# Performance work log

Measured on AMD Instinct MI355X. Metric: run time of the kernel, lower is better.

The kernel has to match this reference:

```python
import jax, jax.numpy as jnp
import numpy as np

NUM_HEADS = 16
HEAD_DIM = 64
NUM_BUCKETS = 32
MAX_DIST = 128
EPS = 1e-5
SCALE = HEAD_DIM ** -0.5


def layer_norm(x, g, b):
    m = jnp.mean(x, axis=-1, keepdims=True)
    v = jnp.mean(jnp.square(x - m), axis=-1, keepdims=True)
    return (x - m) * jax.lax.rsqrt(v + EPS) * g + b


def rel_pos_bias(emb, num_q, num_k):
    # T5-style relative position bucketing (non-causal, bidirectional halves)
    i, j = num_q, num_k
    q_pos = jnp.arange(j - i, j)
    k_pos = jnp.arange(j)
    rel = k_pos[None, :] - q_pos[:, None]  # [i, j]
    nb = NUM_BUCKETS // 2
    ret = (rel >= 0).astype(jnp.int32) * nb
    n = jnp.abs(rel)
    max_exact = nb // 2
    val_large = max_exact + (
        jnp.log(jnp.maximum(n, 1).astype(jnp.float32) / max_exact)
        / np.log(MAX_DIST / max_exact) * (nb - max_exact)
    ).astype(jnp.int32)
    val_large = jnp.minimum(val_large, nb - 1)
    bucket = ret + jnp.where(n < max_exact, n, val_large)
    bias = emb[bucket]                       # [i, j, h]
    return jnp.transpose(bias, (2, 0, 1))[None]  # [1, h, i, j]


def attention(x, ctx, ng, nbv, ncg, ncb, wq, wkv, wo, bo, rel_emb):
    b, n, _ = x.shape
    m = ctx.shape[1]
    xn = layer_norm(x, ng, nbv)
    cn = layer_norm(ctx, ncg, ncb)
    q = xn @ wq                              # [b, n, mid]
    kv = cn @ wkv                            # [b, m, 2*mid]
    k, v = jnp.split(kv, 2, axis=-1)
    def heads(t, L):
        return t.reshape(b, L, NUM_HEADS, HEAD_DIM).transpose(0, 2, 1, 3)
    q, k, v = heads(q, n), heads(k, m), heads(v, m)
    sim = jnp.einsum('bhnd,bhmd->bhnm', q, k)
    sim = (sim + rel_pos_bias(rel_emb, n, m)) * SCALE  # bias added pre-scale (faithful)
    attn = jax.nn.softmax(sim, axis=-1)
    out = jnp.einsum('bhnm,bhmd->bhnd', attn, v)
    out = out.transpose(0, 2, 1, 3).reshape(b, n, NUM_HEADS * HEAD_DIM)
    return out @ wo + bo


def setup_inputs() -> dict:
    key = jax.random.key(0)
    ks = jax.random.split(key, 20)
    F, MID, CF = 1024, NUM_HEADS * HEAD_DIM, 1024
    w = lambda k, shape, s=0.02: jax.random.normal(k, shape, jnp.float32) * s
    inp = {
        'x': jax.random.normal(ks[0], (2, 2048, F), jnp.float32),
        'context': jax.random.normal(ks[1], (2, 512, CF), jnp.float32),
        # self-attention params
        'sa_norm_g': 1.0 + w(ks[2], (F,), 0.1), 'sa_norm_b': w(ks[3], (F,), 0.1),
        'sa_normc_g': 1.0 + w(ks[4], (F,), 0.1), 'sa_normc_b': w(ks[5], (F,), 0.1),
        'sa_wq': w(ks[6], (F, MID)), 'sa_wkv': w(ks[7], (F, 2 * MID)),
        'sa_wo': w(ks[8], (MID, F)), 'sa_bo': w(ks[9], (F,), 0.01),
        'sa_rel': w(ks[10], (NUM_BUCKETS, NUM_HEADS), 0.1),
        # cross-attention params
        'ca_norm_g': 1.0 + w(ks[11], (F,), 0.1), 'ca_norm_b': w(ks[12], (F,), 0.1),
        'ca_normc_g': 1.0 + w(ks[13], (CF,), 0.1), 'ca_normc_b': w(ks[14], (CF,), 0.1),
        'ca_wq': w(ks[15], (F, MID)), 'ca_wkv': w(ks[16], (CF, 2 * MID)),
        'ca_wo': w(ks[17], (MID, F)), 'ca_bo': w(ks[18], (F,), 0.01),
        'ca_rel': w(ks[19], (NUM_BUCKETS, NUM_HEADS), 0.1),
    }
    return inp


def reference(x, context,
              sa_norm_g, sa_norm_b, sa_normc_g, sa_normc_b,
              sa_wq, sa_wkv, sa_wo, sa_bo, sa_rel,
              ca_norm_g, ca_norm_b, ca_normc_g, ca_normc_b,
              ca_wq, ca_wkv, ca_wo, ca_bo, ca_rel):
    # self-attention (context = x, norm_context applied to x)
    x = attention(x, x, sa_norm_g, sa_norm_b, sa_normc_g, sa_normc_b,
                  sa_wq, sa_wkv, sa_wo, sa_bo, sa_rel) + x
    # cross-attention with residual
    x = attention(x, context, ca_norm_g, ca_norm_b, ca_normc_g, ca_normc_b,
                  ca_wq, ca_wkv, ca_wo, ca_bo, ca_rel) + x
    return x
```

## Files before the change

### kernel.cpp

```cpp
#include <hip/hip_runtime.h>
#include <hip/hip_bf16.h>

typedef __hip_bfloat16 bf16;
typedef __attribute__((ext_vector_type(8))) short bf16x8;
typedef __attribute__((ext_vector_type(4))) float f32x4;

__device__ __forceinline__ float b2f(bf16 v) { return __bfloat162float(v); }
__device__ __forceinline__ bf16 f2b(float v) { return __float2bfloat16(v); }

__device__ __forceinline__ float ldx(const void* p, size_t i, bool isb) {
    return isb ? b2f(((const bf16*)p)[i]) : ((const float*)p)[i];
}
__device__ __forceinline__ void stx(void* p, size_t i, bool isb, float v) {
    if (isb) ((bf16*)p)[i] = f2b(v);
    else     ((float*)p)[i] = v;
}
__device__ __forceinline__ void ldx8(const void* p, size_t i, bool isb, float* o) {
    if (isb) {
        const bf16x8 v = *(const bf16x8*)((const bf16*)p + i);
#pragma unroll
        for (int j = 0; j < 8; j++) o[j] = b2f(((const bf16*)&v)[j]);
    } else {
        const float4 v0 = *(const float4*)((const float*)p + i);
        const float4 v1 = *(const float4*)((const float*)p + i + 4);
        o[0]=v0.x; o[1]=v0.y; o[2]=v0.z; o[3]=v0.w;
        o[4]=v1.x; o[5]=v1.y; o[6]=v1.z; o[7]=v1.w;
    }
}

__global__ void sniff_kernel(const void* __restrict__ x, int* __restrict__ flag) {
    const unsigned* w = (const unsigned*)x;
    const int t = threadIdx.x;
    int cnt = 0;
#pragma unroll
    for (int i = 0; i < 4; i++) {
        const unsigned word = w[t * 4 + i];
        const int e = (word >> 23) & 0xFF;
        cnt += (e >= 192) ? 1 : 0;
    }
    __shared__ int red[4];
#pragma unroll
    for (int o = 32; o > 0; o >>= 1) cnt += __shfl_down(cnt, o);
    if ((t & 63) == 0) red[t >> 6] = cnt;
    __syncthreads();
    if (t == 0) flag[0] = ((red[0] + red[1] + red[2] + red[3]) >= 512) ? 1 : 0;
}

__global__ void wconv8_kernel(const void* __restrict__ Wq,
                              const void* __restrict__ Wkv,
                              const void* __restrict__ Wo,
                              const void* __restrict__ Wq2,
                              const void* __restrict__ Wkv2,
                              const void* __restrict__ Wo2,
                              bf16* __restrict__ WTq, bf16* __restrict__ WTkv,
                              bf16* __restrict__ WTo,
                              bf16* __restrict__ WTq2, bf16* __restrict__ WTkv2,
                              bf16* __restrict__ WTo2,
                              const int* __restrict__ flagp) {
    const bool isb = (*flagp != 0);
    const int z = blockIdx.z;
    const int zz = z & 3;
    const bool ca = z >= 4;
    const void* W = ca ? ((zz == 0) ? Wq2 : (zz == 3) ? Wo2 : Wkv2)
                       : ((zz == 0) ? Wq  : (zz == 3) ? Wo  : Wkv);
    bf16* Wt      = ca ? ((zz == 0) ? WTq2 : (zz == 3) ? WTo2 : WTkv2)
                       : ((zz == 0) ? WTq  : (zz == 3) ? WTo  : WTkv);
    const int N   = (zz == 1 || zz == 2) ? 2048 : 1024;
    const int K = 1024;
    __shared__ float T[64][65];
    const int n0 = blockIdx.x * 64 + ((zz == 2) ? 1024 : 0);
    const int k0 = blockIdx.y * 64;
    const int t = threadIdx.x;
    const int rr = t >> 3, c8 = (t & 7) * 8;
#pragma unroll
    for (int i = 0; i < 2; i++) {
        const int row = rr + i * 32;
        float v[8];
        ldx8(W, (size_t)(k0 + row) * N + n0 + c8, isb, v);
#pragma unroll
        for (int j = 0; j < 8; j++) T[row][c8 + j] = v[j];
    }
    __syncthreads();
#pragma unroll
    for (int i = 0; i < 2; i++) {
        const int row = rr + i * 32;
        bf16x8 ov;
#pragma unroll
        for (int j = 0; j < 8; j++) ((bf16*)&ov)[j] = f2b(T[c8 + j][row]);
        *(bf16x8*)(Wt + (size_t)(n0 + row) * K + k0 + c8) = ov;
    }
}

__global__ void ln_dual_kernel(const void* __restrict__ in, size_t in_off, long in_bs,
                               int in_ext,
                               const void* __restrict__ g1, const void* __restrict__ b1,
                               const void* __restrict__ g2, const void* __restrict__ b2,
                               bf16* __restrict__ out1, bf16* __restrict__ out2,
                               long out_bs, const int* __restrict__ flagp) {
    const int F = 1024;
    const bool isb = (*flagp != 0);
    const bool inb = in_ext ? isb : true;
    const int row = blockIdx.x;
    const int z = blockIdx.z;
    const int t = threadIdx.x;
    const size_t base = in_off + (size_t)z * in_bs + (size_t)row * F;
    const size_t obase = (size_t)z * out_bs + (size_t)row * F;

    float v[4];
    float s = 0.f;
#pragma unroll
    for (int i = 0; i < 4; i++) { v[i] = ldx(in, base + t + 256 * i, inb); s += v[i]; }

    __shared__ float red1[4];
    __shared__ float red2[4];
#pragma unroll
    for (int o = 32; o > 0; o >>= 1) s += __shfl_down(s, o);
    if ((t & 63) == 0) red1[t >> 6] = s;
    __syncthreads();
    const float mean = (red1[0] + red1[1] + red1[2] + red1[3]) * (1.0f / F);

    float ss = 0.f;
#pragma unroll
    for (int i = 0; i < 4; i++) { float d = v[i] - mean; ss += d * d; }
#pragma unroll
    for (int o = 32; o > 0; o >>= 1) ss += __shfl_down(ss, o);
    if ((t & 63) == 0) red2[t >> 6] = ss;
    __syncthreads();
    const float var = (red2[0] + red2[1] + red2[2] + red2[3]) * (1.0f / F);
    const float rn = rsqrtf(var + 1e-5f);

#pragma unroll
    for (int i = 0; i < 4; i++) {
        const int idx = t + 256 * i;
        const float nv = (v[i] - mean) * rn;
        out1[obase + idx] = f2b(nv * ldx(g1, idx, isb) + ldx(b1, idx, isb));
        if (out2) out2[obase + idx] = f2b(nv * ldx(g2, idx, isb) + ldx(b2, idx, isb));
    }
}

struct GArgs {
    const bf16* A; const bf16* Bt; void* C;
    const void* bias; const void* res;
    bf16* kb0; bf16* kb1;
    int c_ext, res_ext, N, mode, zsplit, zrows, nbx, nby;
};

__global__ __launch_bounds__(256) void gemm_fused(GArgs ga, GArgs gb, GArgs gc,
                                                  const int* __restrict__ flagp) {
    int bx = (int)blockIdx.x;
    GArgs g;
    if (bx < ga.nbx) { g = ga; }
    else if (bx < ga.nbx + gb.nbx) { g = gb; bx -= ga.nbx; }
    else { g = gc; bx -= ga.nbx + gb.nbx; }
    const int by = (int)blockIdx.y;
    if (by >= g.nby) return;

    const int K = 1024;
    const bool isb = (*flagp != 0);

    __shared__ bf16 As[128][72];
    __shared__ bf16 Bs[128][72];

    const int t = threadIdx.x;
    const int w = t >> 6, lane = t & 63, li = lane & 15, quad = lane >> 4;
    const int wm = (w & 1) * 64, wn = (w >> 1) * 64;
    const int bm = by * 128, bn = bx * 128;

    f32x4 acc[4][4];
#pragma unroll
    for (int mi = 0; mi < 4; mi++)
#pragma unroll
        for (int ni = 0; ni < 4; ni++)
#pragma unroll
            for (int r = 0; r < 4; r++) acc[mi][ni][r] = 0.f;

    for (int k0 = 0; k0 < K; k0 += 64) {
#pragma unroll
        for (int c = 0; c < 4; c++) {
            const int d = c * 256 + t;
            const int row = d >> 3, ch = (d & 7) * 8;
            *(bf16x8*)&As[row][ch] = *(const bf16x8*)(g.A + (size_t)(bm + row) * K + k0 + ch);
            *(bf16x8*)&Bs[row][ch] = *(const bf16x8*)(g.Bt + (size_t)(bn + row) * K + k0 + ch);
        }
        __syncthreads();
#pragma unroll
        for (int kc = 0; kc < 2; kc++) {
            bf16x8 af[4], bfr[4];
#pragma unroll
            for (int i = 0; i < 4; i++) {
                af[i]  = *(const bf16x8*)&As[wm + i * 16 + li][kc * 32 + quad * 8];
                bfr[i] = *(const bf16x8*)&Bs[wn + i * 16 + li][kc * 32 + quad * 8];
            }
#pragma unroll
            for (int mi = 0; mi < 4; mi++)
#pragma unroll
                for (int ni = 0; ni < 4; ni++)
                    acc[mi][ni] = __builtin_amdgcn_mfma_f32_16x16x32_bf16(
                        af[mi], bfr[ni], acc[mi][ni], 0, 0, 0);
        }
        __syncthreads();
    }

    if (g.mode == 1) {
#pragma unroll
        for (int mi = 0; mi < 4; mi++)
#pragma unroll
            for (int r = 0; r < 4; r++) {
                const int row = bm + wm + mi * 16 + quad * 4 + r;
                bf16* kb = (row < g.zsplit) ? g.kb0 : g.kb1;
                const int lrow = (row < g.zsplit) ? row : row - g.zsplit;
#pragma unroll
                for (int ni = 0; ni < 4; ni++) {
                    const int col = bn + wn + ni * 16 + li;
                    const float v = acc[mi][ni][r];
                    if (col < 1024)
                        kb[(size_t)lrow * 1024 + col] = f2b(v);
                    else
                        kb[(size_t)1024 * g.zrows + (size_t)(col - 1024) * g.zrows + lrow] = f2b(v);
                }
            }
        return;
    }

#pragma unroll
    for (int mi = 0; mi < 4; mi++)
#pragma unroll
        for (int r = 0; r < 4; r++) {
            const int row = bm + wm + mi * 16 + quad * 4 + r;
#pragma unroll
            for (int ni = 0; ni < 4; ni++) {
                const int col = bn + wn + ni * 16 + li;
                float v = acc[mi][ni][r];
                if (g.bias) v += ldx(g.bias, col, isb);
                if (g.res)  v += ldx(g.res, (size_t)row * g.N + col, g.res_ext ? isb : true);
                stx(g.C, (size_t)row * g.N + col, g.c_ext ? isb : true, v);
            }
        }
}

__global__ __launch_bounds__(256) void gemm_mfma(
    const bf16* __restrict__ A, long a_bs, const void* __restrict__ W,
    void* __restrict__ C, size_t c_off, long c_bs, int c_ext,
    const void* __restrict__ bias,
    const void* __restrict__ res, size_t res_off, long res_bs, int res_ext,
    int K, int N, int mode, int R,
    bf16* __restrict__ kb0, bf16* __restrict__ kb1,
    const int* __restrict__ flagp) {

    const bool isb = (*flagp != 0);
    const bool resb = res_ext ? isb : true;
    const bool cb = c_ext ? isb : true;
    const int z = blockIdx.z;

    const bf16* Az = A + (size_t)z * a_bs;
    const size_t coz = c_off + (size_t)z * c_bs;
    const size_t roz = res_off + (size_t)z * res_bs;

    __shared__ bf16 As[64][72];
    __shared__ bf16 Bs[64][72];

    const int t = threadIdx.x;
    const int w = t >> 6, lane = t & 63, li = lane & 15, quad = lane >> 4;
    const int wm = (w & 1) * 32, wn = (w >> 1) * 32;
    const int bm = blockIdx.y * 64, bn = blockIdx.x * 64;

    f32x4 acc[2][2];
#pragma unroll
    for (int mi = 0; mi < 2; mi++)
#pragma unroll
        for (int ni = 0; ni < 2; ni++)
#pragma unroll
            for (int r = 0; r < 4; r++) acc[mi][ni][r] = 0.f;

    for (int k0 = 0; k0 < K; k0 += 64) {
#pragma unroll
        for (int c = 0; c < 2; c++) {
            const int lin = t * 16 + c * 8;
            const int row = lin >> 6, kk = lin & 63;
            *(bf16x8*)&As[row][kk] = *(const bf16x8*)(Az + (size_t)(bm + row) * K + k0 + kk);
        }
#pragma unroll
        for (int c = 0; c < 2; c++) {
            const int lin = t * 16 + c * 8;
            const int kk = lin >> 6, n0 = lin & 63;
            float v[8];
            ldx8(W, (size_t)(k0 + kk) * N + bn + n0, isb, v);
            const int st = t & 7;
#pragma unroll
            for (int i = 0; i < 8; i++) {
                const int ii = (i + st) & 7;
                Bs[n0 + ii][kk] = f2b(v[ii]);
            }
        }
        __syncthreads();
#pragma unroll
        for (int kc = 0; kc < 2; kc++) {
            bf16x8 af[2], bfr[2];
#pragma unroll
            for (int mi = 0; mi < 2; mi++)
                af[mi] = *(const bf16x8*)&As[wm + mi * 16 + li][kc * 32 + quad * 8];
#pragma unroll
            for (int ni = 0; ni < 2; ni++)
                bfr[ni] = *(const bf16x8*)&Bs[wn + ni * 16 + li][kc * 32 + quad * 8];
#pragma unroll
            for (int mi = 0; mi < 2; mi++)
#pragma unroll
                for (int ni = 0; ni < 2; ni++)
                    acc[mi][ni] = __builtin_amdgcn_mfma_f32_16x16x32_bf16(
                        af[mi], bfr[ni], acc[mi][ni], 0, 0, 0);
        }
        __syncthreads();
    }

    if (mode == 1) {
        bf16* kb = z ? kb1 : kb0;
#pragma unroll
        for (int mi = 0; mi < 2; mi++)
#pragma unroll
            for (int r = 0; r < 4; r++) {
                const int row = bm + wm + mi * 16 + quad * 4 + r;
#pragma unroll
                for (int ni = 0; ni < 2; ni++) {
                    const int col = bn + wn + ni * 16 + li;
                    const float v = acc[mi][ni][r];
                    if (col < 1024)
                        kb[(size_t)row * 1024 + col] = f2b(v);
                    else
                        kb[(size_t)1024 * R + (size_t)(col - 1024) * R + row] = f2b(v);
                }
            }
        return;
    }

#pragma unroll
    for (int mi = 0; mi < 2; mi++)
#pragma unroll
        for (int r = 0; r < 4; r++) {
            const int row = bm + wm + mi * 16 + quad * 4 + r;
#pragma unroll
            for (int ni = 0; ni < 2; ni++) {
                const int col = bn + wn + ni * 16 + li;
                float v = acc[mi][ni][r];
                if (bias) v += ldx(bias, col, isb);
                if (res)  v += ldx(res, roz + (size_t)row * N + col, resb);
                stx(C, coz + (size_t)row * N + col, cb, v);
            }
        }
}

__global__ __launch_bounds__(64) void attn_flash(
    const bf16* __restrict__ qb, const bf16* __restrict__ kv0,
    const bf16* __restrict__ kv1,
    const void* __restrict__ rel_emb, bf16* __restrict__ out,
    long qo_bs, long out_bs, int m, int rel_off, const int* __restrict__ flagp) {

    const float SC = 0.125f * 1.44269504f;
    const bool isb = (*flagp != 0);
    const int id = blockIdx.x;
    const int xcd = id & 7;
    const int slot = id >> 3;
    const int c = (slot >> 6) * 8 + xcd;
    const int h = c & 15, z = c >> 4;
    const int q0 = (slot & 63) * 32;
    const int t = threadIdx.x;
    const int li = t & 15, quad = t >> 4;

    const bf16* qz = qb + (size_t)z * qo_bs;
    bf16* oz = out + (size_t)z * out_bs;
    const bf16* kb = z ? kv1 : kv0;
    const bf16* vtb = kb + (size_t)m * 1024;

    __shared__ float bias_s[32];
    __shared__ float tab[2080];
    __shared__ bf16 Ps[2][16][40];

    if (t < 32) bias_s[t] = ldx(rel_emb, t * 16 + h, isb) * SC - 40.0f;
    __syncthreads();

    const int tsz = m + 31;
    for (int i = t; i < tsz; i += 64) {
        const int rel = i - 31 - q0 + rel_off;
        const int ab = rel < 0 ? -rel : rel;
        int bucket = rel >= 0 ? 16 : 0;
        if (ab < 8) {
            bucket += ab;
        } else {
            const int p = 31 - __clz(ab);
            const int k2 = 2 * p + ((ab * ab >= (1 << (2 * p + 1))) ? 1 : 0);
            const int val = k2 + 2;
            bucket += (val > 15) ? 15 : val;
        }
        tab[i] = bias_s[bucket];
    }
    __syncthreads();

    bf16x8 aq[2][2];
#pragma unroll
    for (int g = 0; g < 2; g++)
#pragma unroll
        for (int kc = 0; kc < 2; kc++)
            aq[g][kc] = *(const bf16x8*)(qz + (size_t)(q0 + g * 16 + li) * 1024
                                         + h * 64 + kc * 32 + quad * 8);

    bf16x8 ones;
#pragma unroll
    for (int j = 0; j < 8; j++) ((short*)&ones)[j] = 0x3F80;

    f32x4 o[2][4], lac[2];
#pragma unroll
    for (int g = 0; g < 2; g++) {
#pragma unroll
        for (int r = 0; r < 4; r++) lac[g][r] = 0.f;
#pragma unroll
        for (int nb = 0; nb < 4; nb++)
#pragma unroll
            for (int r = 0; r < 4; r++) o[g][nb][r] = 0.f;
    }

#define LOADKV(KF, VF, J)                                                      \
    {                                                                          \
        _Pragma("unroll")                                                      \
        for (int nb = 0; nb < 2; nb++)                                         \
            _Pragma("unroll")                                                  \
            for (int kc = 0; kc < 2; kc++)                                     \
                KF[nb * 2 + kc] = *(const bf16x8*)(                            \
                    kb + (size_t)((J) + nb * 16 + li) * 1024 + h * 64          \
                    + kc * 32 + quad * 8);                                     \
        _Pragma("unroll")                                                      \
        for (int nb = 0; nb < 4; nb++)                                         \
            VF[nb] = *(const bf16x8*)(                                         \
                vtb + (size_t)(h * 64 + nb * 16 + li) * m + (J) + quad * 8);   \
    }

#define ABODY(KF, VF, J0)                                                      \
    {                                                                          \
        _Pragma("unroll")                                                      \
        for (int g = 0; g < 2; g++) {                                          \
            f32x4 s[2];                                                        \
            _Pragma("unroll")                                                  \
            for (int nb = 0; nb < 2; nb++) {                                   \
                f32x4 a;                                                       \
                _Pragma("unroll")                                              \
                for (int r = 0; r < 4; r++) a[r] = 0.f;                        \
                _Pragma("unroll")                                              \
                for (int kc = 0; kc < 2; kc++)                                 \
                    a = __builtin_amdgcn_mfma_f32_16x16x32_bf16(               \
                        aq[g][kc], KF[nb * 2 + kc], a, 0, 0, 0);               \
                s[nb] = a;                                                     \
            }                                                                  \
            _Pragma("unroll")                                                  \
            for (int nb = 0; nb < 2; nb++)                                     \
                _Pragma("unroll")                                              \
                for (int r = 0; r < 4; r++) {                                  \
                    const int ti = (J0) + nb * 16 + li + 31                    \
                                   - (g * 16 + quad * 4 + r);                  \
                    s[nb][r] = exp2f(fmaf(s[nb][r], SC, tab[ti]));             \
                }                                                              \
            _Pragma("unroll")                                                  \
            for (int nb = 0; nb < 2; nb++)                                     \
                _Pragma("unroll")                                              \
                for (int r = 0; r < 4; r++)                                    \
                    Ps[g][quad * 4 + r][nb * 16 + li] = f2b(s[nb][r]);         \
            const bf16x8 ap = *(const bf16x8*)&Ps[g][li][quad * 8];            \
            _Pragma("unroll")                                                  \
            for (int nb = 0; nb < 4; nb++)                                     \
                o[g][nb] = __builtin_amdgcn_mfma_f32_16x16x32_bf16(            \
                    ap, VF[nb], o[g][nb], 0, 0, 0);                            \
            lac[g] = __builtin_amdgcn_mfma_f32_16x16x32_bf16(                  \
                ap, ones, lac[g], 0, 0, 0);                                    \
        }                                                                      \
    }

    bf16x8 kA[4], vA[4], kB[4], vB[4];
    LOADKV(kA, vA, 0);
    for (int j0 = 0; j0 < m; j0 += 64) {
        LOADKV(kB, vB, j0 + 32);
        ABODY(kA, vA, j0);
        const int jn = (j0 + 64 < m) ? (j0 + 64) : 0;
        LOADKV(kA, vA, jn);
        ABODY(kB, vB, j0 + 32);
    }

#undef LOADKV
#undef ABODY

#pragma unroll
    for (int g = 0; g < 2; g++)
#pragma unroll
        for (int r = 0; r < 4; r++) {
            const float inv = 1.0f / lac[g][r];
            const int qi = q0 + g * 16 + quad * 4 + r;
#pragma unroll
            for (int nb = 0; nb < 4; nb++)
                oz[(size_t)qi * 1024 + h * 64 + nb * 16 + li] = f2b(o[g][nb][r] * inv);
        }
}

extern "C" void kernel_launch(void* const* d_in, const int* in_sizes, int n_in,
                              void* d_out, int out_size, void* d_ws, size_t ws_size,
                              hipStream_t stream) {
    const long M1 = 1024 * 1024;
    const long M2 = 2 * 1024 * 1024;
    const long M4 = 4 * 1024 * 1024;
    if (ws_size < 24u * 1024 * 1024 + 256) return;

    const void* x      = d_in[0];
    const void* ctx    = d_in[1];
    const void* sa_ng  = d_in[2];
    const void* sa_nb  = d_in[3];
    const void* sa_ncg = d_in[4];
    const void* sa_ncb = d_in[5];
    const void* sa_wq  = d_in[6];
    const void* sa_wkv = d_in[7];
    const void* sa_wo  = d_in[8];
    const void* sa_bo  = d_in[9];
    const void* sa_rel = d_in[10];
    const void* ca_ng  = d_in[11];
    const void* ca_nb  = d_in[12];
    const void* ca_ncg = d_in[13];
    const void* ca_ncb = d_in[14];
    const void* ca_wq  = d_in[15];
    const void* ca_wkv = d_in[16];
    const void* ca_wo  = d_in[17];
    const void* ca_bo  = d_in[18];
    const void* ca_rel = d_in[19];

    int* flag = (int*)d_ws;
    bf16* F_A = (bf16*)((char*)d_ws + 256);
    bf16* F_B = F_A + M4;
    bf16* F_C = F_B + M4;
    bf16* WT  = F_C + M4;
    bf16* F_X = WT + M4;
    bf16* F_Y = F_X + M4;
    bf16* WT2 = F_Y + 3 * M1;
    bf16* qd  = (bf16*)d_out;

    sniff_kernel<<<1, 256, 0, stream>>>(x, flag);

    if (ws_size >= 56u * 1024 * 1024 + 256) {
        bf16* WTq  = WT;
        bf16* WTkv = WT + M1;
        bf16* WTo  = WT + 3 * M1;
        bf16* WT2q  = WT2;
        bf16* WT2kv = WT2 + M1;
        bf16* WT2o  = WT2 + 3 * M1;
        bf16* CAK0 = F_Y + M1;
        bf16* CAK1 = F_Y + 2 * M1;
        GArgs gz = {};

        wconv8_kernel<<<dim3(16, 16, 8), 256, 0, stream>>>(
            sa_wq, sa_wkv, sa_wo, ca_wq, ca_wkv, ca_wo,
            WTq, WTkv, WTo, WT2q, WT2kv, WT2o, flag);
        ln_dual_kernel<<<dim3(2048, 1, 2), 256, 0, stream>>>(
            x, 0, M2, 1, sa_ng, sa_nb, sa_ncg, sa_ncb, F_X, F_B, M2, flag);
        ln_dual_kernel<<<dim3(512, 1, 2), 256, 0, stream>>>(
            ctx, 0, 512 * 1024, 1, ca_ncg, ca_ncb, nullptr, nullptr,
            F_Y, nullptr, 512 * 1024, flag);

        {
            GArgs gq = {};
            gq.A = F_X; gq.Bt = WTq; gq.C = qd;
            gq.N = 1024; gq.nbx = 8; gq.nby = 32;
            GArgs gkv = {};
            gkv.A = F_B; gkv.Bt = WTkv;
            gkv.N = 2048; gkv.mode = 1; gkv.zsplit = 2048; gkv.zrows = 2048;
            gkv.kb0 = F_A; gkv.kb1 = F_C; gkv.nbx = 16; gkv.nby = 32;
            GArgs gca = {};
            gca.A = F_Y; gca.Bt = WT2kv;
            gca.N = 2048; gca.mode = 1; gca.zsplit = 512; gca.zrows = 512;
            gca.kb0 = CAK0; gca.kb1 = CAK1; gca.nbx = 16; gca.nby = 8;
            gemm_fused<<<dim3(40, 32), 256, 0, stream>>>(gq, gkv, gca, flag);
        }

        attn_flash<<<dim3(2048), 64, 0, stream>>>(
            qd, F_A, F_C, sa_rel, qd, M2, M2, 2048, 0, flag);
        {
            GArgs go = {};
            go.A = qd; go.Bt = WTo; go.C = F_B;
            go.bias = sa_bo; go.res = x; go.res_ext = 1;
            go.N = 1024; go.nbx = 8; go.nby = 32;
            gemm_fused<<<dim3(8, 32), 256, 0, stream>>>(go, gz, gz, flag);
        }

        ln_dual_kernel<<<dim3(2048, 1, 2), 256, 0, stream>>>(
            F_B, 0, M2, 0, ca_ng, ca_nb, nullptr, nullptr, F_X, nullptr, M2, flag);
        {
            GArgs gq = {};
            gq.A = F_X; gq.Bt = WT2q; gq.C = qd;
            gq.N = 1024; gq.nbx = 8; gq.nby = 32;
            gemm_fused<<<dim3(8, 32), 256, 0, stream>>>(gq, gz, gz, flag);
        }
        attn_flash<<<dim3(2048), 64, 0, stream>>>(
            qd, CAK0, CAK1, ca_rel, F_C, M2, M2, 512, 1536, flag);
        {
            GArgs go = {};
            go.A = F_C; go.Bt = WT2o; go.C = d_out; go.c_ext = 1;
            go.bias = ca_bo; go.res = F_B;
            go.N = 1024; go.nbx = 8; go.nby = 32;
            gemm_fused<<<dim3(8, 32), 256, 0, stream>>>(go, gz, gz, flag);
        }
        return;
    }

    ln_dual_kernel<<<dim3(2048, 1, 2), 256, 0, stream>>>(
        x, 0, M2, 1, sa_ng, sa_nb, sa_ncg, sa_ncb, F_A, F_B, M2, flag);
    gemm_mfma<<<dim3(16, 32, 2), 256, 0, stream>>>(
        F_A, M2, sa_wq, qd, 0, M2, 0, nullptr, nullptr, 0, 0, 0,
        1024, 1024, 0, 0, nullptr, nullptr, flag);
    gemm_mfma<<<dim3(32, 32, 2), 256, 0, stream>>>(
        F_B, M2, sa_wkv, nullptr, 0, 0, 0, nullptr, nullptr, 0, 0, 0,
        1024, 2048, 1, 2048, F_A, F_C, flag);
    attn_flash<<<dim3(2048), 64, 0, stream>>>(
        qd, F_A, F_C, sa_rel, qd, M2, M2, 2048, 0, flag);
    gemm_mfma<<<dim3(16, 32, 2), 256, 0, stream>>>(
        qd, M2, sa_wo, F_B, 0, M2, 0, sa_bo, x, 0, M2, 1,
        1024, 1024, 0, 0, nullptr, nullptr, flag);

    ln_dual_kernel<<<dim3(2048, 1, 2), 256, 0, stream>>>(
        F_B, 0, M2, 0, ca_ng, ca_nb, nullptr, nullptr, F_A, nullptr, M2, flag);
    ln_dual_kernel<<<dim3(512, 1, 2), 256, 0, stream>>>(
        ctx, 0, 512 * 1024, 1, ca_ncg, ca_ncb, nullptr, nullptr,
        F_C, nullptr, 512 * 1024, flag);
    gemm_mfma<<<dim3(16, 32, 2), 256, 0, stream>>>(
        F_A, M2, ca_wq, qd, 0, M2, 0, nullptr, nullptr, 0, 0, 0,
        1024, 1024, 0, 0, nullptr, nullptr, flag);
    gemm_mfma<<<dim3(32, 8, 2), 256, 0, stream>>>(
        F_C, 512 * 1024, ca_wkv, nullptr, 0, 0, 0, nullptr, nullptr, 0, 0, 0,
        1024, 2048, 1, 512, F_A, F_A + M1, flag);
    attn_flash<<<dim3(2048), 64, 0, stream>>>(
        qd, F_A, F_A + M1, ca_rel, F_C, M2, M2, 512, 1536, flag);
    gemm_mfma<<<dim3(16, 32, 2), 256, 0, stream>>>(
        F_C, M2, ca_wo, d_out, 0, M2, 1, ca_bo, F_B, 0, M2, 0,
        1024, 1024, 0, 0, nullptr, nullptr, flag);
}
```

Baseline: 489.3 us.

## Split attention over key halves with partial-sum combine kernel

Replaces the single-pass flash attention launches with a split-K variant that processes each half of the key range in separate blocks, writing fp32 partial outputs and row sums to workspace, followed by a combine kernel that sums and normalizes them. This doubles the block count to improve occupancy across CUs. The K/V loop also drops its manual double-buffered prefetch in favor of a simpler single-stage loop with s_setprio around MFMA sections. The cost is extra fp32 partial traffic, an additional launch per attention, and a larger workspace requirement, which may make the fast path fall back if the workspace is smaller.

```diff
diff --git a/kernel.cpp b/kernel.cpp
--- a/kernel.cpp
+++ b/kernel.cpp
@@ -372,7 +372,7 @@
 
     __shared__ float bias_s[32];
     __shared__ float tab[2080];
-    __shared__ bf16 Ps[2][16][40];
+    __shared__ bf16 Ps[16][40];
 
     if (t < 32) bias_s[t] = ldx(rel_emb, t * 16 + h, isb) * SC - 40.0f;
     __syncthreads();
@@ -417,72 +417,57 @@
             for (int r = 0; r < 4; r++) o[g][nb][r] = 0.f;
     }
 
-#define LOADKV(KF, VF, J)                                                      \
-    {                                                                          \
-        _Pragma("unroll")                                                      \
-        for (int nb = 0; nb < 2; nb++)                                         \
-            _Pragma("unroll")                                                  \
-            for (int kc = 0; kc < 2; kc++)                                     \
-                KF[nb * 2 + kc] = *(const bf16x8*)(                            \
-                    kb + (size_t)((J) + nb * 16 + li) * 1024 + h * 64          \
-                    + kc * 32 + quad * 8);                                     \
-        _Pragma("unroll")                                                      \
-        for (int nb = 0; nb < 4; nb++)                                         \
-            VF[nb] = *(const bf16x8*)(                                         \
-                vtb + (size_t)(h * 64 + nb * 16 + li) * m + (J) + quad * 8);   \
-    }
-
-#define ABODY(KF, VF, J0)                                                      \
-    {                                                                          \
-        _Pragma("unroll")                                                      \
-        for (int g = 0; g < 2; g++) {                                          \
-            f32x4 s[2];                                                        \
-            _Pragma("unroll")                                                  \
-            for (int nb = 0; nb < 2; nb++) {                                   \
-                f32x4 a;                                                       \
-                _Pragma("unroll")                                              \
-                for (int r = 0; r < 4; r++) a[r] = 0.f;                        \
-                _Pragma("unroll")                                              \
-                for (int kc = 0; kc < 2; kc++)                                 \
-                    a = __builtin_amdgcn_mfma_f32_16x16x32_bf16(               \
-                        aq[g][kc], KF[nb * 2 + kc], a, 0, 0, 0);               \
-                s[nb] = a;                                                     \
-            }                                                                  \
-            _Pragma("unroll")                                                  \
-            for (int nb = 0; nb < 2; nb++)                                     \
-                _Pragma("unroll")                                              \
-                for (int r = 0; r < 4; r++) {                                  \
-                    const int ti = (J0) + nb * 16 + li + 31                    \
-                                   - (g * 16 + quad * 4 + r);                  \
-                    s[nb][r] = exp2f(fmaf(s[nb][r], SC, tab[ti]));             \
-                }                                                              \
-            _Pragma("unroll")                                                  \
-            for (int nb = 0; nb < 2; nb++)                                     \
-                _Pragma("unroll")                                              \
-                for (int r = 0; r < 4; r++)                                    \
-                    Ps[g][quad * 4 + r][nb * 16 + li] = f2b(s[nb][r]);         \
-            const bf16x8 ap = *(const bf16x8*)&Ps[g][li][quad * 8];            \
-            _Pragma("unroll")                                                  \
-            for (int nb = 0; nb < 4; nb++)                                     \
-                o[g][nb] = __builtin_amdgcn_mfma_f32_16x16x32_bf16(            \
-                    ap, VF[nb], o[g][nb], 0, 0, 0);                            \
-            lac[g] = __builtin_amdgcn_mfma_f32_16x16x32_bf16(                  \
-                ap, ones, lac[g], 0, 0, 0);                                    \
-        }                                                                      \
-    }
-
-    bf16x8 kA[4], vA[4], kB[4], vB[4];
-    LOADKV(kA, vA, 0);
-    for (int j0 = 0; j0 < m; j0 += 64) {
-        LOADKV(kB, vB, j0 + 32);
-        ABODY(kA, vA, j0);
-        const int jn = (j0 + 64 < m) ? (j0 + 64) : 0;
-        LOADKV(kA, vA, jn);
-        ABODY(kB, vB, j0 + 32);
-    }
-
-#undef LOADKV
-#undef ABODY
+    for (int j0 = 0; j0 < m; j0 += 32) {
+        bf16x8 kf[4], vf[4];
+#pragma unroll
+        for (int nb = 0; nb < 2; nb++)
+#pragma unroll
+            for (int kc = 0; kc < 2; kc++)
+                kf[nb * 2 + kc] = *(const bf16x8*)(
+                    kb + (size_t)(j0 + nb * 16 + li) * 1024 + h * 64 + kc * 32 + quad * 8);
+#pragma unroll
+        for (int nb = 0; nb < 4; nb++)
+            vf[nb] = *(const bf16x8*)(
+                vtb + (size_t)(h * 64 + nb * 16 + li) * m + j0 + quad * 8);
+
+#pragma unroll
+        for (int g = 0; g < 2; g++) {
+            f32x4 s[2];
+            __builtin_amdgcn_s_setprio(1);
+#pragma unroll
+            for (int nb = 0; nb < 2; nb++) {
+                f32x4 a;
+#pragma unroll
+                for (int r = 0; r < 4; r++) a[r] = 0.f;
+#pragma unroll
+                for (int kc = 0; kc < 2; kc++)
+                    a = __builtin_amdgcn_mfma_f32_16x16x32_bf16(aq[g][kc], kf[nb * 2 + kc],
+                                                                a, 0, 0, 0);
+                s[nb] = a;
+            }
+            __builtin_amdgcn_s_setprio(0);
+#pragma unroll
+            for (int nb = 0; nb < 2; nb++)
+#pragma unroll
+                for (int r = 0; r < 4; r++) {
+                    const int ti = j0 + nb * 16 + li + 31 - (g * 16 + quad * 4 + r);
+                    s[nb][r] = exp2f(fmaf(s[nb][r], SC, tab[ti]));
+                }
+#pragma unroll
+            for (int nb = 0; nb < 2; nb++)
+#pragma unroll
+                for (int r = 0; r < 4; r++)
+                    Ps[quad * 4 + r][nb * 16 + li] = f2b(s[nb][r]);
+            const bf16x8 ap = *(const bf16x8*)&Ps[li][quad * 8];
+            __builtin_amdgcn_s_setprio(1);
+#pragma unroll
+            for (int nb = 0; nb < 4; nb++)
+                o[g][nb] = __builtin_amdgcn_mfma_f32_16x16x32_bf16(ap, vf[nb],
+                                                                   o[g][nb], 0, 0, 0);
+            lac[g] = __builtin_amdgcn_mfma_f32_16x16x32_bf16(ap, ones, lac[g], 0, 0, 0);
+            __builtin_amdgcn_s_setprio(0);
+        }
+    }
 
 #pragma unroll
     for (int g = 0; g < 2; g++)
@@ -494,6 +479,173 @@
             for (int nb = 0; nb < 4; nb++)
                 oz[(size_t)qi * 1024 + h * 64 + nb * 16 + li] = f2b(o[g][nb][r] * inv);
         }
+}
+
+__global__ __launch_bounds__(64) void attn_split(
+    const bf16* __restrict__ qb, const bf16* __restrict__ kv0,
+    const bf16* __restrict__ kv1,
+    const void* __restrict__ rel_emb,
+    float* __restrict__ po, float* __restrict__ pl,
+    long qo_bs, int m, int rel_off, const int* __restrict__ flagp) {
+
+    const float SC = 0.125f * 1.44269504f;
+    const bool isb = (*flagp != 0);
+    const int id = blockIdx.x;
+    const int xcd = id & 7;
+    const int slot = id >> 3;
+    const int qslot = slot & 63;
+    const int q0 = qslot * 32;
+    const int v = (slot >> 6) * 8 + xcd;
+    const int h = v & 15;
+    const int zh = v >> 4;
+    const int z = zh & 1, half = zh >> 1;
+    const int t = threadIdx.x;
+    const int li = t & 15, quad = t >> 4;
+
+    const int m_h = m >> 1;
+    const int jbeg = half * m_h;
+
+    const bf16* qz = qb + (size_t)z * qo_bs;
+    const bf16* kb = z ? kv1 : kv0;
+    const bf16* vtb = kb + (size_t)m * 1024;
+
+    __shared__ float bias_s[32];
+    __shared__ float tab[1088];
+    __shared__ bf16 Ps[16][40];
+
+    if (t < 32) bias_s[t] = ldx(rel_emb, t * 16 + h, isb) * SC - 40.0f;
+    __syncthreads();
+
+    const int tsz = m_h + 31;
+    for (int i = t; i < tsz; i += 64) {
+        const int j = jbeg + i;
+        const int rel = j - 31 - q0 + rel_off;
+        const int ab = rel < 0 ? -rel : rel;
+        int bucket = rel >= 0 ? 16 : 0;
+        if (ab < 8) {
+            bucket += ab;
+        } else {
+            const int p = 31 - __clz(ab);
+            const int k2 = 2 * p + ((ab * ab >= (1 << (2 * p + 1))) ? 1 : 0);
+            const int val = k2 + 2;
+            bucket += (val > 15) ? 15 : val;
+        }
+        tab[i] = bias_s[bucket];
+    }
+    __syncthreads();
+
+    bf16x8 aq[2][2];
+#pragma unroll
+    for (int g = 0; g < 2; g++)
+#pragma unroll
+        for (int kc = 0; kc < 2; kc++)
+            aq[g][kc] = *(const bf16x8*)(qz + (size_t)(q0 + g * 16 + li) * 1024
+                                         + h * 64 + kc * 32 + quad * 8);
+
+    bf16x8 ones;
+#pragma unroll
+    for (int j = 0; j < 8; j++) ((short*)&ones)[j] = 0x3F80;
+
+    f32x4 o[2][4], lac[2];
+#pragma unroll
+    for (int g = 0; g < 2; g++) {
+#pragma unroll
+        for (int r = 0; r < 4; r++) lac[g][r] = 0.f;
+#pragma unroll
+        for (int nb = 0; nb < 4; nb++)
+#pragma unroll
+            for (int r = 0; r < 4; r++) o[g][nb][r] = 0.f;
+    }
+
+    for (int jl = 0; jl < m_h; jl += 32) {
+        const int j0 = jbeg + jl;
+        bf16x8 kf[4], vf[4];
+#pragma unroll
+        for (int nb = 0; nb < 2; nb++)
+#pragma unroll
+            for (int kc = 0; kc < 2; kc++)
+                kf[nb * 2 + kc] = *(const bf16x8*)(
+                    kb + (size_t)(j0 + nb * 16 + li) * 1024 + h * 64 + kc * 32 + quad * 8);
+#pragma unroll
+        for (int nb = 0; nb < 4; nb++)
+            vf[nb] = *(const bf16x8*)(
+                vtb + (size_t)(h * 64 + nb * 16 + li) * m + j0 + quad * 8);
+
+#pragma unroll
+        for (int g = 0; g < 2; g++) {
+            f32x4 s[2];
+            __builtin_amdgcn_s_setprio(1);
+#pragma unroll
+            for (int nb = 0; nb < 2; nb++) {
+                f32x4 a;
+#pragma unroll
+                for (int r = 0; r < 4; r++) a[r] = 0.f;
+#pragma unroll
+                for (int kc = 0; kc < 2; kc++)
+                    a = __builtin_amdgcn_mfma_f32_16x16x32_bf16(aq[g][kc], kf[nb * 2 + kc],
+                                                                a, 0, 0, 0);
+                s[nb] = a;
+            }
+            __builtin_amdgcn_s_setprio(0);
+#pragma unroll
+            for (int nb = 0; nb < 2; nb++)
+#pragma unroll
+                for (int r = 0; r < 4; r++) {
+                    const int ti = jl + nb * 16 + li + 31 - (g * 16 + quad * 4 + r);
+                    s[nb][r] = exp2f(fmaf(s[nb][r], SC, tab[ti]));
+                }
+#pragma unroll
+            for (int nb = 0; nb < 2; nb++)
+#pragma unroll
+                for (int r = 0; r < 4; r++)
+                    Ps[quad * 4 + r][nb * 16 + li] = f2b(s[nb][r]);
+            const bf16x8 ap = *(const bf16x8*)&Ps[li][quad * 8];
+            __builtin_amdgcn_s_setprio(1);
+#pragma unroll
+            for (int nb = 0; nb < 4; nb++)
+                o[g][nb] = __builtin_amdgcn_mfma_f32_16x16x32_bf16(ap, vf[nb],
+                                                                   o[g][nb], 0, 0, 0);
+            lac[g] = __builtin_amdgcn_mfma_f32_16x16x32_bf16(ap, ones, lac[g], 0, 0, 0);
+            __builtin_amdgcn_s_setprio(0);
+        }
+    }
+
+    const int pidx = ((z * 2 + half) * 16 + h) * 64 + qslot;
+    float* op = po + (size_t)pidx * 2048;
+    float* lp = pl + (size_t)pidx * 32;
+#pragma unroll
+    for (int g = 0; g < 2; g++)
+#pragma unroll
+        for (int r = 0; r < 4; r++) {
+            const int row = g * 16 + quad * 4 + r;
+            if (li == 0) lp[row] = lac[g][r];
+#pragma unroll
+            for (int nb = 0; nb < 4; nb++)
+                op[row * 64 + nb * 16 + li] = o[g][nb][r];
+        }
+}
+
+__global__ __launch_bounds__(64) void attn_comb(
+    const float* __restrict__ po, const float* __restrict__ pl,
+    bf16* __restrict__ out, long out_bs) {
+    const int id = blockIdx.x;
+    const int qslot = id & 63;
+    const int v = id >> 6;
+    const int h = v & 15, z = v >> 4;
+    const int p0 = ((z * 2 + 0) * 16 + h) * 64 + qslot;
+    const int p1 = ((z * 2 + 1) * 16 + h) * 64 + qslot;
+    const float* o0 = po + (size_t)p0 * 2048;
+    const float* o1 = po + (size_t)p1 * 2048;
+    const float* l0 = pl + (size_t)p0 * 32;
+    const float* l1 = pl + (size_t)p1 * 32;
+    bf16* oz = out + (size_t)z * out_bs;
+    const int t = threadIdx.x;
+#pragma unroll 4
+    for (int r = 0; r < 32; r++) {
+        const float inv = 1.0f / (l0[r] + l1[r]);
+        const float val = (o0[r * 64 + t] + o1[r * 64 + t]) * inv;
+        oz[(size_t)(qslot * 32 + r) * 1024 + h * 64 + t] = f2b(val);
+    }
 }
 
 extern "C" void kernel_launch(void* const* d_in, const int* in_sizes, int n_in,
@@ -533,11 +685,13 @@
     bf16* F_X = WT + M4;
     bf16* F_Y = F_X + M4;
     bf16* WT2 = F_Y + 3 * M1;
+    float* P_O = (float*)(WT2 + M4);
+    float* P_L = P_O + 4096 * 2048;
     bf16* qd  = (bf16*)d_out;
 
     sniff_kernel<<<1, 256, 0, stream>>>(x, flag);
 
-    if (ws_size >= 56u * 1024 * 1024 + 256) {
+    if (ws_size >= 96u * 1024 * 1024 + 256) {
         bf16* WTq  = WT;
         bf16* WTkv = WT + M1;
         bf16* WTo  = WT + 3 * M1;
@@ -572,8 +726,9 @@
             gemm_fused<<<dim3(40, 32), 256, 0, stream>>>(gq, gkv, gca, flag);
         }
 
-        attn_flash<<<dim3(2048), 64, 0, stream>>>(
-            qd, F_A, F_C, sa_rel, qd, M2, M2, 2048, 0, flag);
+        attn_split<<<dim3(4096), 64, 0, stream>>>(
+            qd, F_A, F_C, sa_rel, P_O, P_L, M2, 2048, 0, flag);
+        attn_comb<<<dim3(2048), 64, 0, stream>>>(P_O, P_L, qd, M2);
         {
             GArgs go = {};
             go.A = qd; go.Bt = WTo; go.C = F_B;
@@ -590,8 +745,9 @@
             gq.N = 1024; gq.nbx = 8; gq.nby = 32;
             gemm_fused<<<dim3(8, 32), 256, 0, stream>>>(gq, gz, gz, flag);
         }
-        attn_flash<<<dim3(2048), 64, 0, stream>>>(
-            qd, CAK0, CAK1, ca_rel, F_C, M2, M2, 512, 1536, flag);
+        attn_split<<<dim3(4096), 64, 0, stream>>>(
+            qd, CAK0, CAK1, ca_rel, P_O, P_L, M2, 512, 1536, flag);
+        attn_comb<<<dim3(2048), 64, 0, stream>>>(P_O, P_L, F_C, M2);
         {
             GArgs go = {};
             go.A = F_C; go.Bt = WT2o; go.C = d_out; go.c_ext = 1;
```

New measurement: 538.1 us. +10.0%, slower.

## Use direct global-to-LDS loads in fused QKV GEMM and simplify attention loop

Applied to the files above, without the earlier changes.

Adds a GEMM variant that uses global_load_lds to move A and B tiles straight into unpadded shared memory, skipping the register round-trip, and uses it for the fused Q/KV projection launch. The attention kernel drops its manual double-buffered K/V register prefetch and goes back to a simple 32-key loop with one P staging buffer. It also wraps the MFMA sections in s_setprio so waves doing matrix math get priority. Risks: the unpadded 64-wide LDS rows may cause bank conflicts on the fragment reads, and losing the prefetch may expose global load latency in attention.

```diff
diff --git a/kernel.cpp b/kernel.cpp
--- a/kernel.cpp
+++ b/kernel.cpp
@@ -26,6 +26,12 @@
         o[0]=v0.x; o[1]=v0.y; o[2]=v0.z; o[3]=v0.w;
         o[4]=v1.x; o[5]=v1.y; o[6]=v1.z; o[7]=v1.w;
     }
+}
+
+__device__ __forceinline__ void glds16(const void* g, void* l) {
+    __builtin_amdgcn_global_load_lds(
+        (const __attribute__((address_space(1))) void*)g,
+        (__attribute__((address_space(3))) void*)l, 16, 0, 0);
 }
 
 __global__ void sniff_kernel(const void* __restrict__ x, int* __restrict__ flag) {
@@ -145,6 +151,44 @@
     int c_ext, res_ext, N, mode, zsplit, zrows, nbx, nby;
 };
 
+#define GEMM_EPILOGUE                                                          \
+    if (g.mode == 1) {                                                         \
+        _Pragma("unroll")                                                      \
+        for (int mi = 0; mi < 4; mi++)                                         \
+            _Pragma("unroll")                                                  \
+            for (int r = 0; r < 4; r++) {                                      \
+                const int row = bm + wm + mi * 16 + quad * 4 + r;              \
+                bf16* kb = (row < g.zsplit) ? g.kb0 : g.kb1;                   \
+                const int lrow = (row < g.zsplit) ? row : row - g.zsplit;      \
+                _Pragma("unroll")                                              \
+                for (int ni = 0; ni < 4; ni++) {                               \
+                    const int col = bn + wn + ni * 16 + li;                    \
+                    const float v = acc[mi][ni][r];                            \
+                    if (col < 1024)                                            \
+                        kb[(size_t)lrow * 1024 + col] = f2b(v);                \
+                    else                                                       \
+                        kb[(size_t)1024 * g.zrows                              \
+                           + (size_t)(col - 1024) * g.zrows + lrow] = f2b(v);  \
+                }                                                              \
+            }                                                                  \
+        return;                                                                \
+    }                                                                          \
+    _Pragma("unroll")                                                          \
+    for (int mi = 0; mi < 4; mi++)                                             \
+        _Pragma("unroll")                                                      \
+        for (int r = 0; r < 4; r++) {                                          \
+            const int row = bm + wm + mi * 16 + quad * 4 + r;                  \
+            _Pragma("unroll")                                                  \
+            for (int ni = 0; ni < 4; ni++) {                                   \
+                const int col = bn + wn + ni * 16 + li;                        \
+                float v = acc[mi][ni][r];                                      \
+                if (g.bias) v += ldx(g.bias, col, isb);                        \
+                if (g.res)  v += ldx(g.res, (size_t)row * g.N + col,           \
+                                     g.res_ext ? isb : true);                  \
+                stx(g.C, (size_t)row * g.N + col, g.c_ext ? isb : true, v);    \
+            }                                                                  \
+        }
+
 __global__ __launch_bounds__(256) void gemm_fused(GArgs ga, GArgs gb, GArgs gc,
                                                   const int* __restrict__ flagp) {
     int bx = (int)blockIdx.x;
@@ -201,41 +245,68 @@
         __syncthreads();
     }
 
-    if (g.mode == 1) {
-#pragma unroll
-        for (int mi = 0; mi < 4; mi++)
-#pragma unroll
-            for (int r = 0; r < 4; r++) {
-                const int row = bm + wm + mi * 16 + quad * 4 + r;
-                bf16* kb = (row < g.zsplit) ? g.kb0 : g.kb1;
-                const int lrow = (row < g.zsplit) ? row : row - g.zsplit;
-#pragma unroll
-                for (int ni = 0; ni < 4; ni++) {
-                    const int col = bn + wn + ni * 16 + li;
-                    const float v = acc[mi][ni][r];
-                    if (col < 1024)
-                        kb[(size_t)lrow * 1024 + col] = f2b(v);
-                    else
-                        kb[(size_t)1024 * g.zrows + (size_t)(col - 1024) * g.zrows + lrow] = f2b(v);
-                }
+    GEMM_EPILOGUE
+}
+
+__global__ __launch_bounds__(256) void gemm_fused_lds(GArgs ga, GArgs gb, GArgs gc,
+                                                      const int* __restrict__ flagp) {
+    int bx = (int)blockIdx.x;
+    GArgs g;
+    if (bx < ga.nbx) { g = ga; }
+    else if (bx < ga.nbx + gb.nbx) { g = gb; bx -= ga.nbx; }
+    else { g = gc; bx -= ga.nbx + gb.nbx; }
+    const int by = (int)blockIdx.y;
+    if (by >= g.nby) return;
+
+    const int K = 1024;
+    const bool isb = (*flagp != 0);
+
+    __shared__ bf16 As[128][64];
+    __shared__ bf16 Bs[128][64];
+
+    const int t = threadIdx.x;
+    const int w = t >> 6, lane = t & 63, li = lane & 15, quad = lane >> 4;
+    const int wm = (w & 1) * 64, wn = (w >> 1) * 64;
+    const int bm = by * 128, bn = bx * 128;
+    const int srow = t >> 3;
+    const int sch  = (t & 7) * 8;
+
+    f32x4 acc[4][4];
+#pragma unroll
+    for (int mi = 0; mi < 4; mi++)
+#pragma unroll
+        for (int ni = 0; ni < 4; ni++)
+#pragma unroll
+            for (int r = 0; r < 4; r++) acc[mi][ni][r] = 0.f;
+
+    for (int k0 = 0; k0 < K; k0 += 64) {
+#pragma unroll
+        for (int c = 0; c < 4; c++) {
+            glds16(g.A + (size_t)(bm + c * 32 + srow) * K + k0 + sch,
+                   (char*)&As[0][0] + (size_t)(c * 256 + w * 64) * 16);
+            glds16(g.Bt + (size_t)(bn + c * 32 + srow) * K + k0 + sch,
+                   (char*)&Bs[0][0] + (size_t)(c * 256 + w * 64) * 16);
+        }
+        __syncthreads();
+#pragma unroll
+        for (int kc = 0; kc < 2; kc++) {
+            bf16x8 af[4], bfr[4];
+#pragma unroll
+            for (int i = 0; i < 4; i++) {
+                af[i]  = *(const bf16x8*)&As[wm + i * 16 + li][kc * 32 + quad * 8];
+                bfr[i] = *(const bf16x8*)&Bs[wn + i * 16 + li][kc * 32 + quad * 8];
             }
-        return;
-    }
-
-#pragma unroll
-    for (int mi = 0; mi < 4; mi++)
-#pragma unroll
-        for (int r = 0; r < 4; r++) {
-            const int row = bm + wm + mi * 16 + quad * 4 + r;
-#pragma unroll
-            for (int ni = 0; ni < 4; ni++) {
-                const int col = bn + wn + ni * 16 + li;
-                float v = acc[mi][ni][r];
-                if (g.bias) v += ldx(g.bias, col, isb);
-                if (g.res)  v += ldx(g.res, (size_t)row * g.N + col, g.res_ext ? isb : true);
-                stx(g.C, (size_t)row * g.N + col, g.c_ext ? isb : true, v);
-            }
-        }
+#pragma unroll
+            for (int mi = 0; mi < 4; mi++)
+#pragma unroll
+                for (int ni = 0; ni < 4; ni++)
+                    acc[mi][ni] = __builtin_amdgcn_mfma_f32_16x16x32_bf16(
+                        af[mi], bfr[ni], acc[mi][ni], 0, 0, 0);
+        }
+        __syncthreads();
+    }
+
+    GEMM_EPILOGUE
 }
 
 __global__ __launch_bounds__(256) void gemm_mfma(
@@ -372,7 +443,7 @@
 
     __shared__ float bias_s[32];
     __shared__ float tab[2080];
-    __shared__ bf16 Ps[2][16][40];
+    __shared__ bf16 Ps[16][40];
 
     if (t < 32) bias_s[t] = ldx(rel_emb, t * 16 + h, isb) * SC - 40.0f;
     __syncthreads();
@@ -417,72 +488,57 @@
             for (int r = 0; r < 4; r++) o[g][nb][r] = 0.f;
     }
 
-#define LOADKV(KF, VF, J)                                                      \
-    {                                                                          \
-        _Pragma("unroll")                                                      \
-        for (int nb = 0; nb < 2; nb++)                                         \
-            _Pragma("unroll")                                                  \
-            for (int kc = 0; kc < 2; kc++)                                     \
-                KF[nb * 2 + kc] = *(const bf16x8*)(                            \
-                    kb + (size_t)((J) + nb * 16 + li) * 1024 + h * 64          \
-                    + kc * 32 + quad * 8);                                     \
-        _Pragma("unroll")                                                      \
-        for (int nb = 0; nb < 4; nb++)                                         \
-            VF[nb] = *(const bf16x8*)(                                         \
-                vtb + (size_t)(h * 64 + nb * 16 + li) * m + (J) + quad * 8);   \
-    }
-
-#define ABODY(KF, VF, J0)                                                      \
-    {                                                                          \
-        _Pragma("unroll")                                                      \
-        for (int g = 0; g < 2; g++) {                                          \
-            f32x4 s[2];                                                        \
-            _Pragma("unroll")                                                  \
-            for (int nb = 0; nb < 2; nb++) {                                   \
-                f32x4 a;                                                       \
-                _Pragma("unroll")                                              \
-                for (int r = 0; r < 4; r++) a[r] = 0.f;                        \
-                _Pragma("unroll")                                              \
-                for (int kc = 0; kc < 2; kc++)                                 \
-                    a = __builtin_amdgcn_mfma_f32_16x16x32_bf16(               \
-                        aq[g][kc], KF[nb * 2 + kc], a, 0, 0, 0);               \
-                s[nb] = a;                                                     \
-            }                                                                  \
-            _Pragma("unroll")                                                  \
-            for (int nb = 0; nb < 2; nb++)                                     \
-                _Pragma("unroll")                                              \
-                for (int r = 0; r < 4; r++) {                                  \
-                    const int ti = (J0) + nb * 16 + li + 31                    \
-                                   - (g * 16 + quad * 4 + r);                  \
-                    s[nb][r] = exp2f(fmaf(s[nb][r], SC, tab[ti]));             \
-                }                                                              \
-            _Pragma("unroll")                                                  \
-            for (int nb = 0; nb < 2; nb++)                                     \
-                _Pragma("unroll")                                              \
-                for (int r = 0; r < 4; r++)                                    \
-                    Ps[g][quad * 4 + r][nb * 16 + li] = f2b(s[nb][r]);         \
-            const bf16x8 ap = *(const bf16x8*)&Ps[g][li][quad * 8];            \
-            _Pragma("unroll")                                                  \
-            for (int nb = 0; nb < 4; nb++)                                     \
-                o[g][nb] = __builtin_amdgcn_mfma_f32_16x16x32_bf16(            \
-                    ap, VF[nb], o[g][nb], 0, 0, 0);                            \
-            lac[g] = __builtin_amdgcn_mfma_f32_16x16x32_bf16(                  \
-                ap, ones, lac[g], 0, 0, 0);                                    \
-        }                                                                      \
-    }
-
-    bf16x8 kA[4], vA[4], kB[4], vB[4];
-    LOADKV(kA, vA, 0);
-    for (int j0 = 0; j0 < m; j0 += 64) {
-        LOADKV(kB, vB, j0 + 32);
-        ABODY(kA, vA, j0);
-        const int jn = (j0 + 64 < m) ? (j0 + 64) : 0;
-        LOADKV(kA, vA, jn);
-        ABODY(kB, vB, j0 + 32);
-    }
-
-#undef LOADKV
-#undef ABODY
+    for (int j0 = 0; j0 < m; j0 += 32) {
+        bf16x8 kf[4], vf[4];
+#pragma unroll
+        for (int nb = 0; nb < 2; nb++)
+#pragma unroll
+            for (int kc = 0; kc < 2; kc++)
+                kf[nb * 2 + kc] = *(const bf16x8*)(
+                    kb + (size_t)(j0 + nb * 16 + li) * 1024 + h * 64 + kc * 32 + quad * 8);
+#pragma unroll
+        for (int nb = 0; nb < 4; nb++)
+            vf[nb] = *(const bf16x8*)(
+                vtb + (size_t)(h * 64 + nb * 16 + li) * m + j0 + quad * 8);
+
+#pragma unroll
+        for (int g = 0; g < 2; g++) {
+            f32x4 s[2];
+            __builtin_amdgcn_s_setprio(1);
+#pragma unroll
+            for (int nb = 0; nb < 2; nb++) {
+                f32x4 a;
+#pragma unroll
+                for (int r = 0; r < 4; r++) a[r] = 0.f;
+#pragma unroll
+                for (int kc = 0; kc < 2; kc++)
+                    a = __builtin_amdgcn_mfma_f32_16x16x32_bf16(aq[g][kc], kf[nb * 2 + kc],
+                                                                a, 0, 0, 0);
+                s[nb] = a;
+            }
+            __builtin_amdgcn_s_setprio(0);
+#pragma unroll
+            for (int nb = 0; nb < 2; nb++)
+#pragma unroll
+                for (int r = 0; r < 4; r++) {
+                    const int ti = j0 + nb * 16 + li + 31 - (g * 16 + quad * 4 + r);
+                    s[nb][r] = exp2f(fmaf(s[nb][r], SC, tab[ti]));
+                }
+#pragma unroll
+            for (int nb = 0; nb < 2; nb++)
+#pragma unroll
+                for (int r = 0; r < 4; r++)
+                    Ps[quad * 4 + r][nb * 16 + li] = f2b(s[nb][r]);
+            const bf16x8 ap = *(const bf16x8*)&Ps[li][quad * 8];
+            __builtin_amdgcn_s_setprio(1);
+#pragma unroll
+            for (int nb = 0; nb < 4; nb++)
+                o[g][nb] = __builtin_amdgcn_mfma_f32_16x16x32_bf16(ap, vf[nb],
+                                                                   o[g][nb], 0, 0, 0);
+            lac[g] = __builtin_amdgcn_mfma_f32_16x16x32_bf16(ap, ones, lac[g], 0, 0, 0);
+            __builtin_amdgcn_s_setprio(0);
+        }
+    }
 
 #pragma unroll
     for (int g = 0; g < 2; g++)
@@ -569,7 +625,7 @@
             gca.A = F_Y; gca.Bt = WT2kv;
             gca.N = 2048; gca.mode = 1; gca.zsplit = 512; gca.zrows = 512;
             gca.kb0 = CAK0; gca.kb1 = CAK1; gca.nbx = 16; gca.nby = 8;
-            gemm_fused<<<dim3(40, 32), 256, 0, stream>>>(gq, gkv, gca, flag);
+            gemm_fused_lds<<<dim3(40, 32), 256, 0, stream>>>(gq, gkv, gca, flag);
         }
 
         attn_flash<<<dim3(2048), 64, 0, stream>>>(
```

After: 494.6 us. Within noise of the previous version (+1.1%).
